# Optimization experiments

Measured on AMD Instinct MI355X. Metric: run time of the kernel, lower is better.

## Reference

```python
import jax, jax.numpy as jnp
import numpy as np

D_MODEL = 1024
NUM_HEADS = 16
KERNEL_EPS = 1e-4
NORM_STAB = 1e-6


def setup_inputs() -> dict:
    key = jax.random.key(0)
    k1, k2, k3, k4 = jax.random.split(key, 4)
    B, L = 4, 2048
    d_head, m = D_MODEL // NUM_HEADS, 256
    return {
        "query": jax.random.normal(k1, (B, L, D_MODEL), jnp.float32),
        "key": jax.random.normal(k2, (B, L, D_MODEL), jnp.float32),
        "value": jax.random.normal(k3, (B, L, D_MODEL), jnp.float32),
        # random projection matrix (fixed, not learned); original uses orthogonal blocks
        "random_features": jax.random.normal(k4, (d_head, m), jnp.float32),
    }


def _performer_forward(query, key, value, random_features):
    B, L, dm = query.shape
    h = NUM_HEADS
    d = dm // h
    m = random_features.shape[1]

    def split_heads(x):  # [B,L,dm] -> [B,h,L,d]
        return x.reshape(B, L, h, d).transpose(0, 2, 1, 3)

    q, k, v = split_heads(query), split_heads(key), split_heads(value)

    # FAVOR+ exp kernel with stabilizers (matches get_projected_queries_and_keys)
    scale = dm ** -0.25
    q = q * scale
    k = k * scale
    proj_q = jnp.einsum('bhld,dm->bhlm', q, random_features)
    proj_k = jnp.einsum('bhld,dm->bhlm', k, random_features)
    h_q = -0.5 * jnp.sum(q * q, axis=-1, keepdims=True)  # [B,h,L,1]
    h_k = -0.5 * jnp.sum(k * k, axis=-1, keepdims=True)
    q_stab = h_q  # reduce_max over a keepdims size-1 axis == identity (faithful)
    k_stab = jnp.max(h_k)  # global scalar
    q_kernel = jnp.exp(h_q + (proj_q - q_stab))
    k_kernel = jnp.exp(h_k + (proj_k - k_stab))
    nc = m ** -0.5
    q_prime = nc * (q_kernel + KERNEL_EPS)  # [B,h,L,m]
    k_prime = nc * (k_kernel + KERNEL_EPS)

    # Causal linear attention: streaming prefix state instead of [B,h,L,m,d] cumsum
    qp = q_prime.transpose(2, 0, 1, 3)  # [L,B,h,m]
    kp = k_prime.transpose(2, 0, 1, 3)
    vp = v.transpose(2, 0, 1, 3)        # [L,B,h,d]

    def step(carry, inp):
        S, Z = carry                      # S:[B,h,m,d], Z:[B,h,m]
        qt, kt, vt = inp
        S = S + kt[..., :, None] * vt[..., None, :]
        Z = Z + kt
        num = jnp.einsum('bhm,bhmd->bhd', qt, S)
        den = jnp.einsum('bhm,bhm->bh', qt, Z)
        return (S, Z), (num, den)

    S0 = jnp.zeros((B, h, m, d), q_prime.dtype)
    Z0 = jnp.zeros((B, h, m), q_prime.dtype)
    _, (nums, dens) = jax.lax.scan(step, (S0, Z0), (qp, kp, vp))
    nums = nums.transpose(1, 2, 0, 3)          # [B,h,L,d]
    dens = dens.transpose(1, 2, 0)[..., None]  # [B,h,L,1]

    # stabilize denominator near zero (matches _denominator_...)
    extreme = (jnp.abs(dens) <= NORM_STAB).astype(dens.dtype)
    dens = dens + 2.0 * NORM_STAB * extreme
    out = nums / dens

    # merge heads -> [B,L,dm]
    return out.transpose(0, 2, 1, 3).reshape(B, L, dm)


def reference(query, key, value, random_features):
    return _performer_forward(query, key, value, random_features)
```

## Files before the change

kernel.cpp:

```cpp
#include <hip/hip_runtime.h>


#define BB 4
#define HH 16
#define LL 2048
#define DH 64
#define DM 1024
#define MM 256
#define CC 64
#define NCH (LL / CC)

constexpr float SCALE = 0.17677669529663687f;
constexpr float NCF   = 0.0625f;
constexpr float KEPS  = 1e-4f;
constexpr float NCFK  = NCF * KEPS;
constexpr float NSTB  = 1e-6f;

typedef __attribute__((ext_vector_type(8))) short s16x8;
typedef __attribute__((ext_vector_type(4))) float f32x4;

__device__ __forceinline__ float bf2f(unsigned short s) {
  return __uint_as_float(((unsigned)s) << 16);
}
__device__ __forceinline__ unsigned short f2bf(float f) {
  unsigned u = __float_as_uint(f);
  u += 0x7FFFu + ((u >> 16) & 1u);
  return (unsigned short)(u >> 16);
}
__device__ __forceinline__ unsigned enc_key(float f) {
  unsigned u = __float_as_uint(f);
  return (u & 0x80000000u) ? ~u : (u | 0x80000000u);
}
__device__ __forceinline__ float dec_key(unsigned k) {
  unsigned u = (k & 0x80000000u) ? (k & 0x7FFFFFFFu) : ~k;
  return __uint_as_float(u);
}

__global__ __launch_bounds__(256) void kstab_kernel(const float* __restrict__ Kin,
                                                    unsigned int* __restrict__ wsu) {
  int lane = threadIdx.x & 63;
  int wave = threadIdx.x >> 6;
  int base = blockIdx.x * 64 + wave * 16;
  float m = -3.4e38f;
  for (int it = 0; it < 16; ++it) {
    int r = base + it;
    float v = Kin[(size_t)r * 64 + lane];
    float s = v * v;
    #pragma unroll
    for (int off = 32; off; off >>= 1) s += __shfl_xor(s, off, 64);
    float hk = -0.5f * (SCALE * SCALE) * s;
    m = fmaxf(m, hk);
  }
  __shared__ float wmax[4];
  if (lane == 0) wmax[wave] = m;
  __syncthreads();
  if (threadIdx.x == 0) {
    float mm = fmaxf(fmaxf(wmax[0], wmax[1]), fmaxf(wmax[2], wmax[3]));
    atomicMax(wsu, enc_key(mm));
  }
}

__global__ __launch_bounds__(256) void rft_prep(const float* __restrict__ RF,
                                                unsigned short* __restrict__ RFTg) {
  int m = threadIdx.x;
  float rv[64];
  #pragma unroll
  for (int d = 0; d < 64; ++d) rv[d] = RF[d * MM + m];
  unsigned swz = (unsigned)((m & 7) << 4);
  #pragma unroll
  for (int c16 = 0; c16 < 8; ++c16) {
    union { unsigned short u[8]; uint4 v; } pk_;
    #pragma unroll
    for (int i = 0; i < 8; ++i) pk_.u[i] = f2bf(rv[c16 * 8 + i]);
    unsigned byte = (unsigned)(m * 128) + (((unsigned)(c16 * 16)) ^ swz);
    *(uint4*)((char*)RFTg + byte) = pk_.v;
  }
}

__global__ __launch_bounds__(256) void phase1_kernel(const float* __restrict__ Kin,
                                                     const float* __restrict__ Vin,
                                                     const unsigned short* __restrict__ RFTg,
                                                     unsigned short* __restrict__ wsSb,
                                                     float* __restrict__ wsZ,
                                                     const unsigned int* __restrict__ wsu,
                                                     int bh0) {
  __shared__ __align__(16) char lds[45056];
  char* U0  = lds;
  char* KPl = lds + 16384;
  char* VT  = lds + 32768;
  float* Zw = (float*)(lds + 40960);

  int slice = blockIdx.x / NCH;
  int c     = blockIdx.x % NCH;
  int bh = bh0 + slice, b = bh >> 4, h = bh & 15;
  const int t    = threadIdx.x;
  const int lane = t & 63;
  const int w    = t >> 6;
  const int rloc = lane & 15;
  const int kc0  = (lane >> 4) * 8;
  const int arow = 16 * w + rloc;
  const unsigned lgrp16 = (unsigned)((lane >> 4) * 16);
  float kst = dec_key(*wsu);

  const float* krow = Kin + ((size_t)(b * LL + c * CC + arow)) * DM + h * DH;
  s16x8 kfrag[2];
  float ss = 0.f;
  #pragma unroll
  for (int kf = 0; kf < 2; ++kf) {
    float4 ka_ = *(const float4*)(krow + kf * 32 + kc0);
    float4 kb_ = *(const float4*)(krow + kf * 32 + kc0 + 4);
    float ks[8] = {ka_.x, ka_.y, ka_.z, ka_.w, kb_.x, kb_.y, kb_.z, kb_.w};
    #pragma unroll
    for (int i = 0; i < 8; ++i) {
      float kv = ks[i] * SCALE;
      ss += kv * kv;
      kfrag[kf][i] = (short)f2bf(kv);
    }
  }
  ss += __shfl_xor(ss, 16, 64);
  ss += __shfl_xor(ss, 32, 64);
  float hkv = -0.5f * ss;
  float hk4[4];
  #pragma unroll
  for (int r = 0; r < 4; ++r) hk4[r] = __shfl(hkv, (lane >> 4) * 4 + r, 64);

  {
    const float* vbase = Vin + ((size_t)(b * LL + c * CC + w * 16)) * DM + h * DH + lane;
    float vv[16];
    #pragma unroll
    for (int i = 0; i < 16; ++i) vv[i] = vbase[(size_t)i * DM];
    unsigned swz = (unsigned)((lane & 7) << 4);
    #pragma unroll
    for (int q = 0; q < 2; ++q) {
      union { unsigned short u[8]; uint4 v; } pk_;
      #pragma unroll
      for (int i = 0; i < 8; ++i) pk_.u[i] = f2bf(vv[q * 8 + i]);
      unsigned byte = (unsigned)(lane * 128) + (((unsigned)(w * 32 + q * 16)) ^ swz);
      *(uint4*)(VT + byte) = pk_.v;
    }
  }

  for (int h2 = 0; h2 < 2; ++h2) {
    __syncthreads();
    {
      const uint4* src = (const uint4*)(RFTg + (size_t)h2 * 8192);
      uint4* dst = (uint4*)U0;
      #pragma unroll
      for (int r2 = 0; r2 < 4; ++r2) dst[t + 256 * r2] = src[t + 256 * r2];
    }
    __syncthreads();

    f32x4 pk[8];
    #pragma unroll
    for (int i = 0; i < 8; ++i) pk[i] = (f32x4)0.f;
    #pragma unroll
    for (int mt = 0; mt < 8; ++mt) {
      int mloc = mt * 16 + rloc;
      unsigned rbyte = (unsigned)(mloc * 128);
      unsigned swz = (unsigned)((mloc & 7) << 4);
      #pragma unroll
      for (int kf = 0; kf < 2; ++kf) {
        s16x8 bf_ = *(const s16x8*)(U0 + rbyte + (((unsigned)(kf * 64) + lgrp16) ^ swz));
        pk[mt] = __builtin_amdgcn_mfma_f32_16x16x32_bf16(kfrag[kf], bf_, pk[mt], 0, 0, 0);
      }
    }
    #pragma unroll
    for (int mt = 0; mt < 8; ++mt) {
      int mloc = mt * 16 + rloc;
      float zp = 0.f;
      #pragma unroll
      for (int r = 0; r < 4; ++r) {
        int cpos = 16 * w + (lane >> 4) * 4 + r;
        float kpv = NCF * __expf(hk4[r] + pk[mt][r] - kst) + NCFK;
        zp += kpv;
        unsigned byte = (unsigned)(mloc * 128) +
                        (((unsigned)(cpos * 2)) ^ ((unsigned)((mloc & 7) << 4)));
        *(unsigned short*)(KPl + byte) = f2bf(kpv);
      }
      zp += __shfl_xor(zp, 16, 64);
      zp += __shfl_xor(zp, 32, 64);
      if (lane < 16) Zw[w * 256 + h2 * 128 + mt * 16 + lane] = zp;
    }
    __syncthreads();

    f32x4 sacc[8];
    #pragma unroll
    for (int i = 0; i < 8; ++i) sacc[i] = (f32x4)0.f;
    s16x8 af[2];
    {
      int drow = w * 16 + rloc;
      unsigned rbyte = (unsigned)(drow * 128);
      unsigned swz = (unsigned)((drow & 7) << 4);
      #pragma unroll
      for (int kf = 0; kf < 2; ++kf)
        af[kf] = *(const s16x8*)(VT + rbyte + (((unsigned)(kf * 64) + lgrp16) ^ swz));
    }
    #pragma unroll
    for (int mt = 0; mt < 8; ++mt) {
      int mrow = mt * 16 + rloc;
      unsigned rbyte = (unsigned)(mrow * 128);
      unsigned swz = (unsigned)((mrow & 7) << 4);
      #pragma unroll
      for (int kf = 0; kf < 2; ++kf) {
        s16x8 bf_ = *(const s16x8*)(KPl + rbyte + (((unsigned)(kf * 64) + lgrp16) ^ swz));
        sacc[mt] = __builtin_amdgcn_mfma_f32_16x16x32_bf16(af[kf], bf_, sacc[mt], 0, 0, 0);
      }
    }
    unsigned short* sdst = wsSb + (size_t)(slice * NCH + c) * 16384;
    #pragma unroll
    for (int mt = 0; mt < 8; ++mt) {
      #pragma unroll
      for (int r = 0; r < 4; ++r) {
        int d = w * 16 + (lane >> 4) * 4 + r;
        int m = h2 * 128 + mt * 16 + rloc;
        sdst[d * 256 + m] = f2bf(sacc[mt][r]);
      }
    }
  }
  __syncthreads();
  float z = Zw[t] + Zw[256 + t] + Zw[512 + t] + Zw[768 + t];
  wsZ[(size_t)(slice * NCH + c) * MM + t] = z;
}

__global__ __launch_bounds__(256) void scan_kernel(const unsigned short* __restrict__ wsSb,
                                                   unsigned short* __restrict__ wsPb,
                                                   float* __restrict__ wsZ) {
  int slice = blockIdx.x >> 3, part = blockIdx.x & 7;
  const int t = threadIdx.x;
  int d_l = t >> 5, moct = t & 31;
  int d = part * 8 + d_l, m0 = moct * 8;
  int half = m0 >> 7, m_l = m0 & 127;
  const unsigned short* srcb = wsSb + (size_t)slice * NCH * 16384 + d * 256 + m0;
  char* dstb = (char*)wsPb + ((size_t)slice * NCH * 2 + half) * 16384 +
               (unsigned)(d * 256) + (((unsigned)(m_l * 2)) ^ ((unsigned)((d & 7) << 4)));
  float run[8] = {0.f, 0.f, 0.f, 0.f, 0.f, 0.f, 0.f, 0.f};
  for (int c = 0; c < NCH; ++c) {
    uint4 v = *(const uint4*)(srcb + (size_t)c * 16384);
    union { unsigned short u[8]; uint4 q; } o;
    #pragma unroll
    for (int i = 0; i < 8; ++i) o.u[i] = f2bf(run[i]);
    *(uint4*)(dstb + (size_t)c * 32768) = o.q;
    const unsigned short* pv = (const unsigned short*)&v;
    #pragma unroll
    for (int i = 0; i < 8; ++i) run[i] += bf2f(pv[i]);
  }
  if (part == 0) {
    for (int e = t; e < MM; e += 256) {
      float zr = 0.f;
      for (int c = 0; c < NCH; ++c) {
        size_t idx = (size_t)slice * NCH * MM + (size_t)c * MM + e;
        float x = wsZ[idx];
        wsZ[idx] = zr;
        zr += x;
      }
    }
  }
}

__global__ __launch_bounds__(256) void phase3_kernel(const float* __restrict__ Qin,
                                                     const float* __restrict__ Kin,
                                                     const float* __restrict__ Vin,
                                                     const unsigned short* __restrict__ RFTg,
                                                     const unsigned short* __restrict__ wsPb,
                                                     const float* __restrict__ wsZ,
                                                     const unsigned int* __restrict__ wsu,
                                                     float* __restrict__ Out,
                                                     int bh0) {
  __shared__ __align__(16) char lds[50176];
  char* U0  = lds;
  char* QPl = lds + 16384;
  char* KPl = lds + 32768;
  float* ZL = (float*)(lds + 49152);

  int slice = blockIdx.x / NCH;
  int c     = blockIdx.x % NCH;
  int bh = bh0 + slice, b = bh >> 4, h = bh & 15;
  const int t    = threadIdx.x;
  const int lane = t & 63;
  const int w    = t >> 6;

  ZL[t] = wsZ[(size_t)(slice * NCH + c) * MM + t];
  float kst = dec_key(*wsu);

  const int rloc = lane & 15;
  const int kc0  = (lane >> 4) * 8;
  const int arow = 16 * w + rloc;
  const float* qrow = Qin + ((size_t)(b * LL + c * CC + arow)) * DM + h * DH;
  const float* krow = Kin + ((size_t)(b * LL + c * CC + arow)) * DM + h * DH;

  s16x8 qfrag[2], kfrag[2];
  float ss = 0.f;
  #pragma unroll
  for (int kf = 0; kf < 2; ++kf) {
    float4 qa_ = *(const float4*)(qrow + kf * 32 + kc0);
    float4 qb_ = *(const float4*)(qrow + kf * 32 + kc0 + 4);
    float4 ka_ = *(const float4*)(krow + kf * 32 + kc0);
    float4 kb_ = *(const float4*)(krow + kf * 32 + kc0 + 4);
    float qs[8] = {qa_.x, qa_.y, qa_.z, qa_.w, qb_.x, qb_.y, qb_.z, qb_.w};
    float ks[8] = {ka_.x, ka_.y, ka_.z, ka_.w, kb_.x, kb_.y, kb_.z, kb_.w};
    #pragma unroll
    for (int i = 0; i < 8; ++i) {
      float qv = qs[i] * SCALE, kv = ks[i] * SCALE;
      ss += kv * kv;
      qfrag[kf][i] = (short)f2bf(qv);
      kfrag[kf][i] = (short)f2bf(kv);
    }
  }
  ss += __shfl_xor(ss, 16, 64);
  ss += __shfl_xor(ss, 32, 64);
  float hkv = -0.5f * ss;

  f32x4 Aacc[4], Oacc[4];
  #pragma unroll
  for (int i = 0; i < 4; ++i) { Aacc[i] = (f32x4)0.f; Oacc[i] = (f32x4)0.f; }
  float den1[4] = {0.f, 0.f, 0.f, 0.f};
  float den2[4] = {0.f, 0.f, 0.f, 0.f};

  float hk4[4];
  #pragma unroll
  for (int r = 0; r < 4; ++r) hk4[r] = __shfl(hkv, (lane >> 4) * 4 + r, 64);

  const unsigned lgrp16 = (unsigned)((lane >> 4) * 16);

  for (int h2 = 0; h2 < 2; ++h2) {
    __syncthreads();
    {
      const uint4* src = (const uint4*)(RFTg + (size_t)h2 * 8192);
      uint4* dst = (uint4*)U0;
      #pragma unroll
      for (int r2 = 0; r2 < 4; ++r2) dst[t + 256 * r2] = src[t + 256 * r2];
    }
    __syncthreads();

    f32x4 pq[8], pk[8];
    #pragma unroll
    for (int i = 0; i < 8; ++i) { pq[i] = (f32x4)0.f; pk[i] = (f32x4)0.f; }
    #pragma unroll
    for (int mt = 0; mt < 8; ++mt) {
      int mloc = mt * 16 + rloc;
      unsigned rbyte = (unsigned)(mloc * 128);
      unsigned swz = (unsigned)((mloc & 7) << 4);
      #pragma unroll
      for (int kf = 0; kf < 2; ++kf) {
        s16x8 bf_ = *(const s16x8*)(U0 + rbyte + (((unsigned)(kf * 64) + lgrp16) ^ swz));
        pq[mt] = __builtin_amdgcn_mfma_f32_16x16x32_bf16(qfrag[kf], bf_, pq[mt], 0, 0, 0);
        pk[mt] = __builtin_amdgcn_mfma_f32_16x16x32_bf16(kfrag[kf], bf_, pk[mt], 0, 0, 0);
      }
    }
    #pragma unroll
    for (int mt = 0; mt < 8; ++mt) {
      int mloc = mt * 16 + rloc;
      #pragma unroll
      for (int r = 0; r < 4; ++r) {
        int row = 16 * w + (lane >> 4) * 4 + r;
        float qpv = NCF * __expf(pq[mt][r]) + NCFK;
        float kpv = NCF * __expf(hk4[r] + pk[mt][r] - kst) + NCFK;
        unsigned byte = (unsigned)(row * 256) +
                        (((unsigned)(mloc * 2)) ^ ((unsigned)((row & 7) << 4)));
        *(unsigned short*)(QPl + byte) = f2bf(qpv);
        *(unsigned short*)(KPl + byte) = f2bf(kpv);
        den2[r] += qpv * ZL[h2 * 128 + mloc];
      }
    }
    __syncthreads();

    uint4 stmp[4];
    {
      const char* ssrc = (const char*)wsPb + ((size_t)(slice * NCH + c) * 2 + h2) * 16384;
      #pragma unroll
      for (int r2 = 0; r2 < 4; ++r2)
        stmp[r2] = *(const uint4*)(ssrc + t * 16 + r2 * 4096);
    }

    s16x8 qa[4];
    {
      unsigned rbyte = (unsigned)(arow * 256);
      unsigned swz = (unsigned)((arow & 7) << 4);
      #pragma unroll
      for (int kf = 0; kf < 4; ++kf)
        qa[kf] = *(const s16x8*)(QPl + rbyte + (((unsigned)(kf * 64) + lgrp16) ^ swz));
    }
    for (int ct = 0; ct <= w; ++ct) {
      int rowb = ct * 16 + rloc;
      unsigned rbyte = (unsigned)(rowb * 256);
      unsigned swz = (unsigned)((rowb & 7) << 4);
      #pragma unroll
      for (int kf = 0; kf < 4; ++kf) {
        s16x8 bf_ = *(const s16x8*)(KPl + rbyte + (((unsigned)(kf * 64) + lgrp16) ^ swz));
        Aacc[ct] = __builtin_amdgcn_mfma_f32_16x16x32_bf16(qa[kf], bf_, Aacc[ct], 0, 0, 0);
      }
    }
    {
      uint4* u0v = (uint4*)U0;
      #pragma unroll
      for (int r2 = 0; r2 < 4; ++r2) u0v[t + 256 * r2] = stmp[r2];
    }
    __syncthreads();

    #pragma unroll
    for (int ct = 0; ct < 4; ++ct) {
      int rowb = ct * 16 + rloc;
      unsigned rbyte = (unsigned)(rowb * 256);
      unsigned swz = (unsigned)((rowb & 7) << 4);
      #pragma unroll
      for (int kf = 0; kf < 4; ++kf) {
        s16x8 bf_ = *(const s16x8*)(U0 + rbyte + (((unsigned)(kf * 64) + lgrp16) ^ swz));
        Oacc[ct] = __builtin_amdgcn_mfma_f32_16x16x32_bf16(qa[kf], bf_, Oacc[ct], 0, 0, 0);
      }
    }
  }

  __syncthreads();

  #pragma unroll
  for (int ct = 0; ct < 4; ++ct) {
    #pragma unroll
    for (int r = 0; r < 4; ++r) {
      int row = 16 * w + (lane >> 4) * 4 + r;
      int col = ct * 16 + rloc;
      float av = (ct <= w && col <= row) ? Aacc[ct][r] : 0.f;
      den1[r] += av;
      unsigned byte = (unsigned)(row * 128) +
                      (((unsigned)(col * 2)) ^ ((unsigned)((row & 7) << 4)));
      *(unsigned short*)(U0 + byte) = f2bf(av);
    }
  }
  {
    const float* vbase = Vin + ((size_t)(b * LL + c * CC + w * 16)) * DM + h * DH + lane;
    float vv[16];
    #pragma unroll
    for (int i = 0; i < 16; ++i) vv[i] = vbase[(size_t)i * DM];
    unsigned swz = (unsigned)((lane & 7) << 4);
    #pragma unroll
    for (int q = 0; q < 2; ++q) {
      union { unsigned short u[8]; uint4 v; } pk_;
      #pragma unroll
      for (int i = 0; i < 8; ++i) pk_.u[i] = f2bf(vv[q * 8 + i]);
      unsigned byte = 8192u + (unsigned)(lane * 128) + (((unsigned)(w * 32 + q * 16)) ^ swz);
      *(uint4*)(U0 + byte) = pk_.v;
    }
  }
  __syncthreads();

  {
    int nkf = (w >= 2) ? 2 : 1;
    unsigned arbyte = (unsigned)(arow * 128);
    unsigned aswz = (unsigned)((arow & 7) << 4);
    for (int kf = 0; kf < nkf; ++kf) {
      s16x8 af = *(const s16x8*)(U0 + arbyte + (((unsigned)(kf * 64) + lgrp16) ^ aswz));
      #pragma unroll
      for (int ct = 0; ct < 4; ++ct) {
        int rowv = ct * 16 + rloc;
        unsigned byte = 8192u + (unsigned)(rowv * 128) +
                        (((unsigned)(kf * 64) + lgrp16) ^ ((unsigned)((rowv & 7) << 4)));
        s16x8 vf = *(const s16x8*)(U0 + byte);
        Oacc[ct] = __builtin_amdgcn_mfma_f32_16x16x32_bf16(af, vf, Oacc[ct], 0, 0, 0);
      }
    }
  }

  float inv[4];
  #pragma unroll
  for (int r = 0; r < 4; ++r) {
    float dv = den1[r] + den2[r];
    dv += __shfl_xor(dv, 1, 64);
    dv += __shfl_xor(dv, 2, 64);
    dv += __shfl_xor(dv, 4, 64);
    dv += __shfl_xor(dv, 8, 64);
    if (fabsf(dv) <= NSTB) dv += 2.f * NSTB;
    inv[r] = 1.0f / dv;
  }
  #pragma unroll
  for (int r = 0; r < 4; ++r) {
    int row = 16 * w + (lane >> 4) * 4 + r;
    size_t g = ((size_t)(b * LL + c * CC + row)) * DM + h * DH;
    #pragma unroll
    for (int ct = 0; ct < 4; ++ct) {
      Out[g + ct * 16 + rloc] = Oacc[ct][r] * inv[r];
    }
  }
}

extern "C" void kernel_launch(void* const* d_in, const int* in_sizes, int n_in,
                              void* d_out, int out_size, void* d_ws, size_t ws_size,
                              hipStream_t stream) {
  const float* Q  = (const float*)d_in[0];
  const float* K  = (const float*)d_in[1];
  const float* V  = (const float*)d_in[2];
  const float* RF = (const float*)d_in[3];
  float* Out = (float*)d_out;
  unsigned int* wsu = (unsigned int*)d_ws;

  const size_t RESV = 1024;
  const size_t RFTB = 32768;
  const size_t perSlice = (size_t)NCH * 16384 * 2
                        + (size_t)NCH * 2 * 16384
                        + (size_t)NCH * MM * 4;
  int G = BB * HH;
  while (G > 1 && RESV + RFTB + (size_t)G * perSlice > ws_size) G >>= 1;

  unsigned short* RFTg = (unsigned short*)((char*)d_ws + RESV);
  unsigned short* wsSb = (unsigned short*)((char*)d_ws + RESV + RFTB);
  unsigned short* wsPb = wsSb + (size_t)G * NCH * 16384;
  float* wsZ = (float*)((char*)wsPb + (size_t)G * NCH * 2 * 16384);

  hipMemsetAsync(d_ws, 0, 4, stream);
  hipLaunchKernelGGL(kstab_kernel, dim3(2048), dim3(256), 0, stream, K, wsu);
  hipLaunchKernelGGL(rft_prep, dim3(1), dim3(256), 0, stream, RF, RFTg);
  for (int bh0 = 0; bh0 < BB * HH; bh0 += G) {
    hipLaunchKernelGGL(phase1_kernel, dim3(G * NCH), dim3(256), 0, stream,
                       K, V, RFTg, wsSb, wsZ, wsu, bh0);
    hipLaunchKernelGGL(scan_kernel, dim3(G * 8), dim3(256), 0, stream, wsSb, wsPb, wsZ);
    hipLaunchKernelGGL(phase3_kernel, dim3(G * NCH), dim3(256), 0, stream,
                       Q, K, V, RFTg, wsPb, wsZ, wsu, Out, bh0);
  }
}
```

Measured before the change: 163.5 us.

## Restructure chunked scan into 8-segment two-level prefix with in-block state carry

Phase 1 now processes four chunks per block and accumulates per-segment KV state in registers, writing one state per segment instead of one per chunk. The scan runs across only eight segments, and phase 3 carries the running state through its four chunks with in-register MFMA updates. The per-bh group loop is dropped, leaving a single launch of each kernel. This cuts workspace traffic and the size of the scan. In exchange, parallelism drops (448 and 512 blocks), phase 3 carries more work serially, and LDS per block is larger.

```diff
diff --git a/kernel.cpp b/kernel.cpp
--- a/kernel.cpp
+++ b/kernel.cpp
@@ -8,7 +8,9 @@
 #define DM 1024
 #define MM 256
 #define CC 64
-#define NCH (LL / CC)
+#define NCH 32
+#define SEGC 4
+#define NSEG 8
 
 constexpr float SCALE = 0.17677669529663687f;
 constexpr float NCF   = 0.0625f;
@@ -77,406 +79,441 @@
   }
 }
 
-__global__ __launch_bounds__(256) void phase1_kernel(const float* __restrict__ Kin,
-                                                     const float* __restrict__ Vin,
-                                                     const unsigned short* __restrict__ RFTg,
-                                                     unsigned short* __restrict__ wsSb,
-                                                     float* __restrict__ wsZ,
-                                                     const unsigned int* __restrict__ wsu,
-                                                     int bh0) {
-  __shared__ __align__(16) char lds[45056];
-  char* U0  = lds;
-  char* KPl = lds + 16384;
-  char* VT  = lds + 32768;
-  float* Zw = (float*)(lds + 40960);
-
-  int slice = blockIdx.x / NCH;
-  int c     = blockIdx.x % NCH;
-  int bh = bh0 + slice, b = bh >> 4, h = bh & 15;
-  const int t    = threadIdx.x;
-  const int lane = t & 63;
-  const int w    = t >> 6;
-  const int rloc = lane & 15;
-  const int kc0  = (lane >> 4) * 8;
+__global__ __launch_bounds__(256, 2) void phase1_kernel(const float* __restrict__ Kin,
+                                                        const float* __restrict__ Vin,
+                                                        const unsigned short* __restrict__ RFTg,
+                                                        unsigned short* __restrict__ wsSeg,
+                                                        float* __restrict__ wsZ,
+                                                        const unsigned int* __restrict__ wsu) {
+  __shared__ __align__(16) char lds[77824];
+  char* RFTl = lds;
+  char* KPmc = lds + 32768;
+  char* VT   = lds + 65536;
+  float* Zw  = (float*)(lds + 73728);
+
+  int slice = blockIdx.x / 7, seg = blockIdx.x % 7;
+  int b = slice >> 4, h = slice & 15;
+  const int t = threadIdx.x, lane = t & 63, w = t >> 6;
+  const int rloc = lane & 15, kc0 = (lane >> 4) * 8;
+  const unsigned lgrp16 = (unsigned)((lane >> 4) * 16);
+  float kst = dec_key(*wsu);
+
+  {
+    const uint4* src = (const uint4*)RFTg;
+    uint4* dst = (uint4*)RFTl;
+    #pragma unroll
+    for (int i = 0; i < 8; ++i) dst[t + 256 * i] = src[t + 256 * i];
+  }
+  #pragma unroll
+  for (int i = 0; i < 4; ++i) Zw[t + 256 * i] = 0.f;
+
+  f32x4 sacc[2][8];
+  #pragma unroll
+  for (int a = 0; a < 2; ++a)
+    #pragma unroll
+    for (int m = 0; m < 8; ++m) sacc[a][m] = (f32x4)0.f;
+
+  for (int cc = 0; cc < SEGC; ++cc) {
+    int c = seg * SEGC + cc;
+    const int arow = 16 * w + rloc;
+    const float* krow = Kin + ((size_t)(b * LL + c * CC + arow)) * DM + h * DH;
+    s16x8 kfrag[2];
+    float ss = 0.f;
+    #pragma unroll
+    for (int kf = 0; kf < 2; ++kf) {
+      float4 ka_ = *(const float4*)(krow + kf * 32 + kc0);
+      float4 kb_ = *(const float4*)(krow + kf * 32 + kc0 + 4);
+      float ks[8] = {ka_.x, ka_.y, ka_.z, ka_.w, kb_.x, kb_.y, kb_.z, kb_.w};
+      #pragma unroll
+      for (int i = 0; i < 8; ++i) {
+        float kv = ks[i] * SCALE;
+        ss += kv * kv;
+        kfrag[kf][i] = (short)f2bf(kv);
+      }
+    }
+    ss += __shfl_xor(ss, 16, 64);
+    ss += __shfl_xor(ss, 32, 64);
+    float hkv = -0.5f * ss;
+    float hk4[4];
+    #pragma unroll
+    for (int r = 0; r < 4; ++r) hk4[r] = __shfl(hkv, (lane >> 4) * 4 + r, 64);
+
+    const float* vbase = Vin + ((size_t)(b * LL + c * CC + w * 16)) * DM + h * DH + lane;
+    float vv[16];
+    #pragma unroll
+    for (int i = 0; i < 16; ++i) vv[i] = vbase[(size_t)i * DM];
+
+    __syncthreads();
+    {
+      unsigned vswz = (unsigned)((lane & 7) << 4);
+      #pragma unroll
+      for (int q = 0; q < 2; ++q) {
+        union { unsigned short u[8]; uint4 v; } pk_;
+        #pragma unroll
+        for (int i = 0; i < 8; ++i) pk_.u[i] = f2bf(vv[q * 8 + i]);
+        unsigned byte = (unsigned)(lane * 128) + (((unsigned)(w * 32 + q * 16)) ^ vswz);
+        *(uint4*)(VT + byte) = pk_.v;
+      }
+    }
+    __syncthreads();
+
+    #pragma unroll
+    for (int h2 = 0; h2 < 2; ++h2) {
+      #pragma unroll
+      for (int mt = 0; mt < 8; ++mt) {
+        int mloc = mt * 16 + rloc;
+        unsigned rbyte = (unsigned)((h2 * 128 + mloc) * 128);
+        unsigned swz = (unsigned)((mloc & 7) << 4);
+        f32x4 pk = (f32x4)0.f;
+        #pragma unroll
+        for (int kf = 0; kf < 2; ++kf) {
+          s16x8 bf_ = *(const s16x8*)(RFTl + rbyte + (((unsigned)(kf * 64) + lgrp16) ^ swz));
+          pk = __builtin_amdgcn_mfma_f32_16x16x32_bf16(kfrag[kf], bf_, pk, 0, 0, 0);
+        }
+        float zp = 0.f;
+        ushort4 kp4;
+        #pragma unroll
+        for (int r = 0; r < 4; ++r) {
+          float kpv = NCF * __expf(hk4[r] + pk[r] - kst) + NCFK;
+          zp += kpv;
+          (&kp4.x)[r] = f2bf(kpv);
+        }
+        int cb = 16 * w + (lane >> 4) * 4;
+        *(ushort4*)(KPmc + h2 * 16384 + mloc * 128 +
+                    (((unsigned)(cb * 2)) ^ ((unsigned)((mloc & 7) << 4)))) = kp4;
+        zp += __shfl_xor(zp, 16, 64);
+        zp += __shfl_xor(zp, 32, 64);
+        if (lane < 16) Zw[w * 256 + h2 * 128 + mt * 16 + lane] += zp;
+      }
+    }
+    __syncthreads();
+
+    s16x8 vt2[2];
+    {
+      int drow = w * 16 + rloc;
+      unsigned rb = (unsigned)(drow * 128), sz = (unsigned)((drow & 7) << 4);
+      #pragma unroll
+      for (int kf = 0; kf < 2; ++kf)
+        vt2[kf] = *(const s16x8*)(VT + rb + (((unsigned)(kf * 64) + lgrp16) ^ sz));
+    }
+    #pragma unroll
+    for (int h2 = 0; h2 < 2; ++h2) {
+      #pragma unroll
+      for (int mt = 0; mt < 8; ++mt) {
+        int mrow = mt * 16 + rloc;
+        unsigned rb = (unsigned)(h2 * 16384 + mrow * 128);
+        unsigned sz = (unsigned)((mrow & 7) << 4);
+        #pragma unroll
+        for (int kf = 0; kf < 2; ++kf) {
+          s16x8 bf_ = *(const s16x8*)(KPmc + rb + (((unsigned)(kf * 64) + lgrp16) ^ sz));
+          sacc[h2][mt] = __builtin_amdgcn_mfma_f32_16x16x32_bf16(vt2[kf], bf_, sacc[h2][mt], 0, 0, 0);
+        }
+      }
+    }
+  }
+
+  {
+    char* sb = (char*)wsSeg + (size_t)(slice * NSEG + seg) * 32768;
+    #pragma unroll
+    for (int j = 0; j < 8; ++j) {
+      int h2 = j >> 2, m0 = (j & 3) * 2;
+      union { unsigned short u[8]; uint4 v; } o;
+      #pragma unroll
+      for (int r = 0; r < 4; ++r) {
+        o.u[r]     = f2bf(sacc[h2][m0][r]);
+        o.u[4 + r] = f2bf(sacc[h2][m0 + 1][r]);
+      }
+      *(uint4*)(sb + (size_t)(j * 256 + t) * 16) = o.v;
+    }
+  }
+  __syncthreads();
+  float z = Zw[t] + Zw[256 + t] + Zw[512 + t] + Zw[768 + t];
+  wsZ[(size_t)(slice * NSEG + seg) * 256 + t] = z;
+}
+
+__global__ __launch_bounds__(256) void scan_kernel(unsigned short* __restrict__ wsSeg,
+                                                   float* __restrict__ wsZ) {
+  int slice = blockIdx.x >> 2, part = blockIdx.x & 3;
+  const int t = threadIdx.x;
+  #pragma unroll
+  for (int rep = 0; rep < 2; ++rep) {
+    int g = part * 512 + rep * 256 + t;
+    char* base = (char*)wsSeg + (size_t)slice * NSEG * 32768 + (size_t)g * 16;
+    float run[8] = {0.f, 0.f, 0.f, 0.f, 0.f, 0.f, 0.f, 0.f};
+    for (int s = 0; s < NSEG; ++s) {
+      char* p = base + (size_t)s * 32768;
+      uint4 x = make_uint4(0, 0, 0, 0);
+      if (s < NSEG - 1) x = *(const uint4*)p;
+      union { unsigned short u[8]; uint4 v; } o;
+      #pragma unroll
+      for (int i = 0; i < 8; ++i) o.u[i] = f2bf(run[i]);
+      *(uint4*)p = o.v;
+      const unsigned short* xu = (const unsigned short*)&x;
+      #pragma unroll
+      for (int i = 0; i < 8; ++i) run[i] += bf2f(xu[i]);
+    }
+  }
+  if (part == 0) {
+    float zr = 0.f;
+    for (int s = 0; s < NSEG; ++s) {
+      float* p = wsZ + ((size_t)slice * NSEG + s) * 256 + t;
+      float x = (s < NSEG - 1) ? *p : 0.f;
+      *p = zr;
+      zr += x;
+    }
+  }
+}
+
+__global__ __launch_bounds__(256, 2) void phase3_kernel(const float* __restrict__ Qin,
+                                                        const float* __restrict__ Kin,
+                                                        const float* __restrict__ Vin,
+                                                        const unsigned short* __restrict__ RFTg,
+                                                        const unsigned short* __restrict__ wsSeg,
+                                                        const float* __restrict__ wsZ,
+                                                        const unsigned int* __restrict__ wsu,
+                                                        float* __restrict__ Out) {
+  __shared__ __align__(16) char lds[78848];
+  char* U0   = lds;
+  char* QP   = lds + 16384;
+  char* KPcm = lds + 32768;
+  char* KPmc = lds + 49152;
+  char* VT   = lds + 65536;
+  float* Zw  = (float*)(lds + 73728);
+  float* ZL  = (float*)(lds + 77824);
+
+  int slice = blockIdx.x >> 3, seg = blockIdx.x & 7;
+  int b = slice >> 4, h = slice & 15;
+  const int t = threadIdx.x, lane = t & 63, w = t >> 6;
+  const int rloc = lane & 15, kc0 = (lane >> 4) * 8;
   const int arow = 16 * w + rloc;
   const unsigned lgrp16 = (unsigned)((lane >> 4) * 16);
   float kst = dec_key(*wsu);
-
-  const float* krow = Kin + ((size_t)(b * LL + c * CC + arow)) * DM + h * DH;
-  s16x8 kfrag[2];
-  float ss = 0.f;
-  #pragma unroll
-  for (int kf = 0; kf < 2; ++kf) {
-    float4 ka_ = *(const float4*)(krow + kf * 32 + kc0);
-    float4 kb_ = *(const float4*)(krow + kf * 32 + kc0 + 4);
-    float ks[8] = {ka_.x, ka_.y, ka_.z, ka_.w, kb_.x, kb_.y, kb_.z, kb_.w};
-    #pragma unroll
-    for (int i = 0; i < 8; ++i) {
-      float kv = ks[i] * SCALE;
-      ss += kv * kv;
-      kfrag[kf][i] = (short)f2bf(kv);
-    }
-  }
-  ss += __shfl_xor(ss, 16, 64);
-  ss += __shfl_xor(ss, 32, 64);
-  float hkv = -0.5f * ss;
-  float hk4[4];
-  #pragma unroll
-  for (int r = 0; r < 4; ++r) hk4[r] = __shfl(hkv, (lane >> 4) * 4 + r, 64);
-
+  int slab = slice * NSEG + seg;
+
+  ZL[t] = wsZ[(size_t)slab * 256 + t];
+
+  f32x4 sacc[2][8];
   {
+    const char* sb = (const char*)wsSeg + (size_t)slab * 32768;
+    #pragma unroll
+    for (int j = 0; j < 8; ++j) {
+      uint4 x = *(const uint4*)(sb + (size_t)(j * 256 + t) * 16);
+      const unsigned short* xu = (const unsigned short*)&x;
+      int h2 = j >> 2, m0 = (j & 3) * 2;
+      #pragma unroll
+      for (int r = 0; r < 4; ++r) {
+        sacc[h2][m0][r]     = bf2f(xu[r]);
+        sacc[h2][m0 + 1][r] = bf2f(xu[4 + r]);
+      }
+    }
+  }
+
+  for (int cc = 0; cc < SEGC; ++cc) {
+    int c = seg * SEGC + cc;
+    const float* qrow = Qin + ((size_t)(b * LL + c * CC + arow)) * DM + h * DH;
+    const float* krow = Kin + ((size_t)(b * LL + c * CC + arow)) * DM + h * DH;
+    s16x8 qfrag[2], kfrag[2];
+    float ss = 0.f;
+    #pragma unroll
+    for (int kf = 0; kf < 2; ++kf) {
+      float4 qa_ = *(const float4*)(qrow + kf * 32 + kc0);
+      float4 qb_ = *(const float4*)(qrow + kf * 32 + kc0 + 4);
+      float4 ka_ = *(const float4*)(krow + kf * 32 + kc0);
+      float4 kb_ = *(const float4*)(krow + kf * 32 + kc0 + 4);
+      float qs[8] = {qa_.x, qa_.y, qa_.z, qa_.w, qb_.x, qb_.y, qb_.z, qb_.w};
+      float ks[8] = {ka_.x, ka_.y, ka_.z, ka_.w, kb_.x, kb_.y, kb_.z, kb_.w};
+      #pragma unroll
+      for (int i = 0; i < 8; ++i) {
+        float qv = qs[i] * SCALE, kv = ks[i] * SCALE;
+        ss += kv * kv;
+        qfrag[kf][i] = (short)f2bf(qv);
+        kfrag[kf][i] = (short)f2bf(kv);
+      }
+    }
+    ss += __shfl_xor(ss, 16, 64);
+    ss += __shfl_xor(ss, 32, 64);
+    float hkv = -0.5f * ss;
+    float hk4[4];
+    #pragma unroll
+    for (int r = 0; r < 4; ++r) hk4[r] = __shfl(hkv, (lane >> 4) * 4 + r, 64);
+
     const float* vbase = Vin + ((size_t)(b * LL + c * CC + w * 16)) * DM + h * DH + lane;
     float vv[16];
     #pragma unroll
     for (int i = 0; i < 16; ++i) vv[i] = vbase[(size_t)i * DM];
-    unsigned swz = (unsigned)((lane & 7) << 4);
-    #pragma unroll
-    for (int q = 0; q < 2; ++q) {
-      union { unsigned short u[8]; uint4 v; } pk_;
-      #pragma unroll
-      for (int i = 0; i < 8; ++i) pk_.u[i] = f2bf(vv[q * 8 + i]);
-      unsigned byte = (unsigned)(lane * 128) + (((unsigned)(w * 32 + q * 16)) ^ swz);
-      *(uint4*)(VT + byte) = pk_.v;
-    }
-  }
-
-  for (int h2 = 0; h2 < 2; ++h2) {
+
+    f32x4 Aacc[4], Oacc[4];
+    #pragma unroll
+    for (int i = 0; i < 4; ++i) { Aacc[i] = (f32x4)0.f; Oacc[i] = (f32x4)0.f; }
+    float den1[4] = {0.f, 0.f, 0.f, 0.f};
+    float den2[4] = {0.f, 0.f, 0.f, 0.f};
+
+    for (int h2 = 0; h2 < 2; ++h2) {
+      __syncthreads();
+      if (h2 == 0) {
+        unsigned vswz = (unsigned)((lane & 7) << 4);
+        #pragma unroll
+        for (int q = 0; q < 2; ++q) {
+          union { unsigned short u[8]; uint4 v; } pk_;
+          #pragma unroll
+          for (int i = 0; i < 8; ++i) pk_.u[i] = f2bf(vv[q * 8 + i]);
+          unsigned byte = (unsigned)(lane * 128) + (((unsigned)(w * 32 + q * 16)) ^ vswz);
+          *(uint4*)(VT + byte) = pk_.v;
+        }
+      }
+      {
+        const uint4* src = (const uint4*)RFTg + h2 * 1024;
+        uint4* dst = (uint4*)U0;
+        #pragma unroll
+        for (int i = 0; i < 4; ++i) dst[t + 256 * i] = src[t + 256 * i];
+      }
+      __syncthreads();
+
+      #pragma unroll
+      for (int mt = 0; mt < 8; ++mt) {
+        int mloc = mt * 16 + rloc;
+        unsigned rbyte = (unsigned)(mloc * 128);
+        unsigned swz = (unsigned)((mloc & 7) << 4);
+        f32x4 pq = (f32x4)0.f, pk = (f32x4)0.f;
+        #pragma unroll
+        for (int kf = 0; kf < 2; ++kf) {
+          s16x8 bf_ = *(const s16x8*)(U0 + rbyte + (((unsigned)(kf * 64) + lgrp16) ^ swz));
+          pq = __builtin_amdgcn_mfma_f32_16x16x32_bf16(qfrag[kf], bf_, pq, 0, 0, 0);
+          pk = __builtin_amdgcn_mfma_f32_16x16x32_bf16(kfrag[kf], bf_, pk, 0, 0, 0);
+        }
+        float zlv = ZL[h2 * 128 + mloc];
+        float zp = 0.f;
+        ushort4 kp4;
+        #pragma unroll
+        for (int r = 0; r < 4; ++r) {
+          int row = 16 * w + (lane >> 4) * 4 + r;
+          float qpv = NCF * __expf(pq[r]) + NCFK;
+          float kpv = NCF * __expf(hk4[r] + pk[r] - kst) + NCFK;
+          den2[r] += qpv * zlv;
+          zp += kpv;
+          (&kp4.x)[r] = f2bf(kpv);
+          unsigned rswz = (unsigned)((row & 7) << 4);
+          *(unsigned short*)(QP + row * 256 + (((unsigned)(mloc * 2)) ^ rswz)) = f2bf(qpv);
+          *(unsigned short*)(KPcm + row * 256 + (((unsigned)(mloc * 2)) ^ rswz)) = f2bf(kpv);
+        }
+        int cb = 16 * w + (lane >> 4) * 4;
+        *(ushort4*)(KPmc + mloc * 128 + (((unsigned)(cb * 2)) ^ ((unsigned)((mloc & 7) << 4)))) = kp4;
+        zp += __shfl_xor(zp, 16, 64);
+        zp += __shfl_xor(zp, 32, 64);
+        if (lane < 16) Zw[w * 256 + h2 * 128 + mt * 16 + lane] = zp;
+      }
+      __syncthreads();
+
+      s16x8 qa[4];
+      {
+        unsigned rb = (unsigned)(arow * 256), sz = (unsigned)((arow & 7) << 4);
+        #pragma unroll
+        for (int kf = 0; kf < 4; ++kf)
+          qa[kf] = *(const s16x8*)(QP + rb + (((unsigned)(kf * 64) + lgrp16) ^ sz));
+      }
+      for (int ct = 0; ct <= w; ++ct) {
+        int rowb = ct * 16 + rloc;
+        unsigned rb = (unsigned)(rowb * 256), sz = (unsigned)((rowb & 7) << 4);
+        #pragma unroll
+        for (int kf = 0; kf < 4; ++kf) {
+          s16x8 bf_ = *(const s16x8*)(KPcm + rb + (((unsigned)(kf * 64) + lgrp16) ^ sz));
+          Aacc[ct] = __builtin_amdgcn_mfma_f32_16x16x32_bf16(qa[kf], bf_, Aacc[ct], 0, 0, 0);
+        }
+      }
+      #pragma unroll
+      for (int mt = 0; mt < 8; ++mt) {
+        int mloc = mt * 16 + rloc;
+        #pragma unroll
+        for (int r = 0; r < 4; ++r) {
+          int d = 16 * w + (lane >> 4) * 4 + r;
+          *(unsigned short*)(U0 + d * 256 +
+                             (((unsigned)(mloc * 2)) ^ ((unsigned)((d & 7) << 4)))) =
+              f2bf(sacc[h2][mt][r]);
+        }
+      }
+      if (cc != SEGC - 1) {
+        s16x8 vt2[2];
+        {
+          int drow = w * 16 + rloc;
+          unsigned rb = (unsigned)(drow * 128), sz = (unsigned)((drow & 7) << 4);
+          #pragma unroll
+          for (int kf = 0; kf < 2; ++kf)
+            vt2[kf] = *(const s16x8*)(VT + rb + (((unsigned)(kf * 64) + lgrp16) ^ sz));
+        }
+        #pragma unroll
+        for (int mt = 0; mt < 8; ++mt) {
+          int mrow = mt * 16 + rloc;
+          unsigned rb = (unsigned)(mrow * 128), sz = (unsigned)((mrow & 7) << 4);
+          #pragma unroll
+          for (int kf = 0; kf < 2; ++kf) {
+            s16x8 bf_ = *(const s16x8*)(KPmc + rb + (((unsigned)(kf * 64) + lgrp16) ^ sz));
+            sacc[h2][mt] = __builtin_amdgcn_mfma_f32_16x16x32_bf16(vt2[kf], bf_, sacc[h2][mt], 0, 0, 0);
+          }
+        }
+      }
+      __syncthreads();
+      #pragma unroll
+      for (int ct = 0; ct < 4; ++ct) {
+        int rowb = ct * 16 + rloc;
+        unsigned rb = (unsigned)(rowb * 256), sz = (unsigned)((rowb & 7) << 4);
+        #pragma unroll
+        for (int kf = 0; kf < 4; ++kf) {
+          s16x8 bf_ = *(const s16x8*)(U0 + rb + (((unsigned)(kf * 64) + lgrp16) ^ sz));
+          Oacc[ct] = __builtin_amdgcn_mfma_f32_16x16x32_bf16(qa[kf], bf_, Oacc[ct], 0, 0, 0);
+        }
+      }
+    }
+
     __syncthreads();
-    {
-      const uint4* src = (const uint4*)(RFTg + (size_t)h2 * 8192);
-      uint4* dst = (uint4*)U0;
-      #pragma unroll
-      for (int r2 = 0; r2 < 4; ++r2) dst[t + 256 * r2] = src[t + 256 * r2];
-    }
-    __syncthreads();
-
-    f32x4 pk[8];
-    #pragma unroll
-    for (int i = 0; i < 8; ++i) pk[i] = (f32x4)0.f;
-    #pragma unroll
-    for (int mt = 0; mt < 8; ++mt) {
-      int mloc = mt * 16 + rloc;
-      unsigned rbyte = (unsigned)(mloc * 128);
-      unsigned swz = (unsigned)((mloc & 7) << 4);
-      #pragma unroll
-      for (int kf = 0; kf < 2; ++kf) {
-        s16x8 bf_ = *(const s16x8*)(U0 + rbyte + (((unsigned)(kf * 64) + lgrp16) ^ swz));
-        pk[mt] = __builtin_amdgcn_mfma_f32_16x16x32_bf16(kfrag[kf], bf_, pk[mt], 0, 0, 0);
-      }
-    }
-    #pragma unroll
-    for (int mt = 0; mt < 8; ++mt) {
-      int mloc = mt * 16 + rloc;
-      float zp = 0.f;
-      #pragma unroll
-      for (int r = 0; r < 4; ++r) {
-        int cpos = 16 * w + (lane >> 4) * 4 + r;
-        float kpv = NCF * __expf(hk4[r] + pk[mt][r] - kst) + NCFK;
-        zp += kpv;
-        unsigned byte = (unsigned)(mloc * 128) +
-                        (((unsigned)(cpos * 2)) ^ ((unsigned)((mloc & 7) << 4)));
-        *(unsigned short*)(KPl + byte) = f2bf(kpv);
-      }
-      zp += __shfl_xor(zp, 16, 64);
-      zp += __shfl_xor(zp, 32, 64);
-      if (lane < 16) Zw[w * 256 + h2 * 128 + mt * 16 + lane] = zp;
-    }
-    __syncthreads();
-
-    f32x4 sacc[8];
-    #pragma unroll
-    for (int i = 0; i < 8; ++i) sacc[i] = (f32x4)0.f;
-    s16x8 af[2];
-    {
-      int drow = w * 16 + rloc;
-      unsigned rbyte = (unsigned)(drow * 128);
-      unsigned swz = (unsigned)((drow & 7) << 4);
-      #pragma unroll
-      for (int kf = 0; kf < 2; ++kf)
-        af[kf] = *(const s16x8*)(VT + rbyte + (((unsigned)(kf * 64) + lgrp16) ^ swz));
-    }
-    #pragma unroll
-    for (int mt = 0; mt < 8; ++mt) {
-      int mrow = mt * 16 + rloc;
-      unsigned rbyte = (unsigned)(mrow * 128);
-      unsigned swz = (unsigned)((mrow & 7) << 4);
-      #pragma unroll
-      for (int kf = 0; kf < 2; ++kf) {
-        s16x8 bf_ = *(const s16x8*)(KPl + rbyte + (((unsigned)(kf * 64) + lgrp16) ^ swz));
-        sacc[mt] = __builtin_amdgcn_mfma_f32_16x16x32_bf16(af[kf], bf_, sacc[mt], 0, 0, 0);
-      }
-    }
-    unsigned short* sdst = wsSb + (size_t)(slice * NCH + c) * 16384;
-    #pragma unroll
-    for (int mt = 0; mt < 8; ++mt) {
-      #pragma unroll
-      for (int r = 0; r < 4; ++r) {
-        int d = w * 16 + (lane >> 4) * 4 + r;
-        int m = h2 * 128 + mt * 16 + rloc;
-        sdst[d * 256 + m] = f2bf(sacc[mt][r]);
-      }
-    }
-  }
-  __syncthreads();
-  float z = Zw[t] + Zw[256 + t] + Zw[512 + t] + Zw[768 + t];
-  wsZ[(size_t)(slice * NCH + c) * MM + t] = z;
-}
-
-__global__ __launch_bounds__(256) void scan_kernel(const unsigned short* __restrict__ wsSb,
-                                                   unsigned short* __restrict__ wsPb,
-                                                   float* __restrict__ wsZ) {
-  int slice = blockIdx.x >> 3, part = blockIdx.x & 7;
-  const int t = threadIdx.x;
-  int d_l = t >> 5, moct = t & 31;
-  int d = part * 8 + d_l, m0 = moct * 8;
-  int half = m0 >> 7, m_l = m0 & 127;
-  const unsigned short* srcb = wsSb + (size_t)slice * NCH * 16384 + d * 256 + m0;
-  char* dstb = (char*)wsPb + ((size_t)slice * NCH * 2 + half) * 16384 +
-               (unsigned)(d * 256) + (((unsigned)(m_l * 2)) ^ ((unsigned)((d & 7) << 4)));
-  float run[8] = {0.f, 0.f, 0.f, 0.f, 0.f, 0.f, 0.f, 0.f};
-  for (int c = 0; c < NCH; ++c) {
-    uint4 v = *(const uint4*)(srcb + (size_t)c * 16384);
-    union { unsigned short u[8]; uint4 q; } o;
-    #pragma unroll
-    for (int i = 0; i < 8; ++i) o.u[i] = f2bf(run[i]);
-    *(uint4*)(dstb + (size_t)c * 32768) = o.q;
-    const unsigned short* pv = (const unsigned short*)&v;
-    #pragma unroll
-    for (int i = 0; i < 8; ++i) run[i] += bf2f(pv[i]);
-  }
-  if (part == 0) {
-    for (int e = t; e < MM; e += 256) {
-      float zr = 0.f;
-      for (int c = 0; c < NCH; ++c) {
-        size_t idx = (size_t)slice * NCH * MM + (size_t)c * MM + e;
-        float x = wsZ[idx];
-        wsZ[idx] = zr;
-        zr += x;
-      }
-    }
-  }
-}
-
-__global__ __launch_bounds__(256) void phase3_kernel(const float* __restrict__ Qin,
-                                                     const float* __restrict__ Kin,
-                                                     const float* __restrict__ Vin,
-                                                     const unsigned short* __restrict__ RFTg,
-                                                     const unsigned short* __restrict__ wsPb,
-                                                     const float* __restrict__ wsZ,
-                                                     const unsigned int* __restrict__ wsu,
-                                                     float* __restrict__ Out,
-                                                     int bh0) {
-  __shared__ __align__(16) char lds[50176];
-  char* U0  = lds;
-  char* QPl = lds + 16384;
-  char* KPl = lds + 32768;
-  float* ZL = (float*)(lds + 49152);
-
-  int slice = blockIdx.x / NCH;
-  int c     = blockIdx.x % NCH;
-  int bh = bh0 + slice, b = bh >> 4, h = bh & 15;
-  const int t    = threadIdx.x;
-  const int lane = t & 63;
-  const int w    = t >> 6;
-
-  ZL[t] = wsZ[(size_t)(slice * NCH + c) * MM + t];
-  float kst = dec_key(*wsu);
-
-  const int rloc = lane & 15;
-  const int kc0  = (lane >> 4) * 8;
-  const int arow = 16 * w + rloc;
-  const float* qrow = Qin + ((size_t)(b * LL + c * CC + arow)) * DM + h * DH;
-  const float* krow = Kin + ((size_t)(b * LL + c * CC + arow)) * DM + h * DH;
-
-  s16x8 qfrag[2], kfrag[2];
-  float ss = 0.f;
-  #pragma unroll
-  for (int kf = 0; kf < 2; ++kf) {
-    float4 qa_ = *(const float4*)(qrow + kf * 32 + kc0);
-    float4 qb_ = *(const float4*)(qrow + kf * 32 + kc0 + 4);
-    float4 ka_ = *(const float4*)(krow + kf * 32 + kc0);
-    float4 kb_ = *(const float4*)(krow + kf * 32 + kc0 + 4);
-    float qs[8] = {qa_.x, qa_.y, qa_.z, qa_.w, qb_.x, qb_.y, qb_.z, qb_.w};
-    float ks[8] = {ka_.x, ka_.y, ka_.z, ka_.w, kb_.x, kb_.y, kb_.z, kb_.w};
-    #pragma unroll
-    for (int i = 0; i < 8; ++i) {
-      float qv = qs[i] * SCALE, kv = ks[i] * SCALE;
-      ss += kv * kv;
-      qfrag[kf][i] = (short)f2bf(qv);
-      kfrag[kf][i] = (short)f2bf(kv);
-    }
-  }
-  ss += __shfl_xor(ss, 16, 64);
-  ss += __shfl_xor(ss, 32, 64);
-  float hkv = -0.5f * ss;
-
-  f32x4 Aacc[4], Oacc[4];
-  #pragma unroll
-  for (int i = 0; i < 4; ++i) { Aacc[i] = (f32x4)0.f; Oacc[i] = (f32x4)0.f; }
-  float den1[4] = {0.f, 0.f, 0.f, 0.f};
-  float den2[4] = {0.f, 0.f, 0.f, 0.f};
-
-  float hk4[4];
-  #pragma unroll
-  for (int r = 0; r < 4; ++r) hk4[r] = __shfl(hkv, (lane >> 4) * 4 + r, 64);
-
-  const unsigned lgrp16 = (unsigned)((lane >> 4) * 16);
-
-  for (int h2 = 0; h2 < 2; ++h2) {
-    __syncthreads();
-    {
-      const uint4* src = (const uint4*)(RFTg + (size_t)h2 * 8192);
-      uint4* dst = (uint4*)U0;
-      #pragma unroll
-      for (int r2 = 0; r2 < 4; ++r2) dst[t + 256 * r2] = src[t + 256 * r2];
-    }
-    __syncthreads();
-
-    f32x4 pq[8], pk[8];
-    #pragma unroll
-    for (int i = 0; i < 8; ++i) { pq[i] = (f32x4)0.f; pk[i] = (f32x4)0.f; }
-    #pragma unroll
-    for (int mt = 0; mt < 8; ++mt) {
-      int mloc = mt * 16 + rloc;
-      unsigned rbyte = (unsigned)(mloc * 128);
-      unsigned swz = (unsigned)((mloc & 7) << 4);
-      #pragma unroll
-      for (int kf = 0; kf < 2; ++kf) {
-        s16x8 bf_ = *(const s16x8*)(U0 + rbyte + (((unsigned)(kf * 64) + lgrp16) ^ swz));
-        pq[mt] = __builtin_amdgcn_mfma_f32_16x16x32_bf16(qfrag[kf], bf_, pq[mt], 0, 0, 0);
-        pk[mt] = __builtin_amdgcn_mfma_f32_16x16x32_bf16(kfrag[kf], bf_, pk[mt], 0, 0, 0);
-      }
-    }
-    #pragma unroll
-    for (int mt = 0; mt < 8; ++mt) {
-      int mloc = mt * 16 + rloc;
+    #pragma unroll
+    for (int ct = 0; ct < 4; ++ct) {
       #pragma unroll
       for (int r = 0; r < 4; ++r) {
         int row = 16 * w + (lane >> 4) * 4 + r;
-        float qpv = NCF * __expf(pq[mt][r]) + NCFK;
-        float kpv = NCF * __expf(hk4[r] + pk[mt][r] - kst) + NCFK;
-        unsigned byte = (unsigned)(row * 256) +
-                        (((unsigned)(mloc * 2)) ^ ((unsigned)((row & 7) << 4)));
-        *(unsigned short*)(QPl + byte) = f2bf(qpv);
-        *(unsigned short*)(KPl + byte) = f2bf(kpv);
-        den2[r] += qpv * ZL[h2 * 128 + mloc];
-      }
-    }
+        int col = ct * 16 + rloc;
+        float av = (ct <= w && col <= row) ? Aacc[ct][r] : 0.f;
+        den1[r] += av;
+        *(unsigned short*)(U0 + row * 128 +
+                           (((unsigned)(col * 2)) ^ ((unsigned)((row & 7) << 4)))) = f2bf(av);
+      }
+    }
+    if (cc != SEGC - 1) ZL[t] += Zw[t] + Zw[256 + t] + Zw[512 + t] + Zw[768 + t];
     __syncthreads();
 
-    uint4 stmp[4];
     {
-      const char* ssrc = (const char*)wsPb + ((size_t)(slice * NCH + c) * 2 + h2) * 16384;
-      #pragma unroll
-      for (int r2 = 0; r2 < 4; ++r2)
-        stmp[r2] = *(const uint4*)(ssrc + t * 16 + r2 * 4096);
-    }
-
-    s16x8 qa[4];
-    {
-      unsigned rbyte = (unsigned)(arow * 256);
-      unsigned swz = (unsigned)((arow & 7) << 4);
-      #pragma unroll
-      for (int kf = 0; kf < 4; ++kf)
-        qa[kf] = *(const s16x8*)(QPl + rbyte + (((unsigned)(kf * 64) + lgrp16) ^ swz));
-    }
-    for (int ct = 0; ct <= w; ++ct) {
-      int rowb = ct * 16 + rloc;
-      unsigned rbyte = (unsigned)(rowb * 256);
-      unsigned swz = (unsigned)((rowb & 7) << 4);
-      #pragma unroll
-      for (int kf = 0; kf < 4; ++kf) {
-        s16x8 bf_ = *(const s16x8*)(KPl + rbyte + (((unsigned)(kf * 64) + lgrp16) ^ swz));
-        Aacc[ct] = __builtin_amdgcn_mfma_f32_16x16x32_bf16(qa[kf], bf_, Aacc[ct], 0, 0, 0);
-      }
-    }
-    {
-      uint4* u0v = (uint4*)U0;
-      #pragma unroll
-      for (int r2 = 0; r2 < 4; ++r2) u0v[t + 256 * r2] = stmp[r2];
-    }
-    __syncthreads();
-
-    #pragma unroll
-    for (int ct = 0; ct < 4; ++ct) {
-      int rowb = ct * 16 + rloc;
-      unsigned rbyte = (unsigned)(rowb * 256);
-      unsigned swz = (unsigned)((rowb & 7) << 4);
-      #pragma unroll
-      for (int kf = 0; kf < 4; ++kf) {
-        s16x8 bf_ = *(const s16x8*)(U0 + rbyte + (((unsigned)(kf * 64) + lgrp16) ^ swz));
-        Oacc[ct] = __builtin_amdgcn_mfma_f32_16x16x32_bf16(qa[kf], bf_, Oacc[ct], 0, 0, 0);
-      }
-    }
-  }
-
-  __syncthreads();
-
-  #pragma unroll
-  for (int ct = 0; ct < 4; ++ct) {
+      int nkf = (w >= 2) ? 2 : 1;
+      unsigned arb = (unsigned)(arow * 128), asz = (unsigned)((arow & 7) << 4);
+      for (int kf = 0; kf < nkf; ++kf) {
+        s16x8 af = *(const s16x8*)(U0 + arb + (((unsigned)(kf * 64) + lgrp16) ^ asz));
+        #pragma unroll
+        for (int ct = 0; ct < 4; ++ct) {
+          int rowv = ct * 16 + rloc;
+          s16x8 vf = *(const s16x8*)(VT + rowv * 128 +
+                                     (((unsigned)(kf * 64) + lgrp16) ^ ((unsigned)((rowv & 7) << 4))));
+          Oacc[ct] = __builtin_amdgcn_mfma_f32_16x16x32_bf16(af, vf, Oacc[ct], 0, 0, 0);
+        }
+      }
+    }
+
+    float inv[4];
+    #pragma unroll
+    for (int r = 0; r < 4; ++r) {
+      float dv = den1[r] + den2[r];
+      dv += __shfl_xor(dv, 1, 64);
+      dv += __shfl_xor(dv, 2, 64);
+      dv += __shfl_xor(dv, 4, 64);
+      dv += __shfl_xor(dv, 8, 64);
+      if (fabsf(dv) <= NSTB) dv += 2.f * NSTB;
+      inv[r] = 1.0f / dv;
+    }
     #pragma unroll
     for (int r = 0; r < 4; ++r) {
       int row = 16 * w + (lane >> 4) * 4 + r;
-      int col = ct * 16 + rloc;
-      float av = (ct <= w && col <= row) ? Aacc[ct][r] : 0.f;
-      den1[r] += av;
-      unsigned byte = (unsigned)(row * 128) +
-                      (((unsigned)(col * 2)) ^ ((unsigned)((row & 7) << 4)));
-      *(unsigned short*)(U0 + byte) = f2bf(av);
-    }
-  }
-  {
-    const float* vbase = Vin + ((size_t)(b * LL + c * CC + w * 16)) * DM + h * DH + lane;
-    float vv[16];
-    #pragma unroll
-    for (int i = 0; i < 16; ++i) vv[i] = vbase[(size_t)i * DM];
-    unsigned swz = (unsigned)((lane & 7) << 4);
-    #pragma unroll
-    for (int q = 0; q < 2; ++q) {
-      union { unsigned short u[8]; uint4 v; } pk_;
-      #pragma unroll
-      for (int i = 0; i < 8; ++i) pk_.u[i] = f2bf(vv[q * 8 + i]);
-      unsigned byte = 8192u + (unsigned)(lane * 128) + (((unsigned)(w * 32 + q * 16)) ^ swz);
-      *(uint4*)(U0 + byte) = pk_.v;
-    }
-  }
-  __syncthreads();
-
-  {
-    int nkf = (w >= 2) ? 2 : 1;
-    unsigned arbyte = (unsigned)(arow * 128);
-    unsigned aswz = (unsigned)((arow & 7) << 4);
-    for (int kf = 0; kf < nkf; ++kf) {
-      s16x8 af = *(const s16x8*)(U0 + arbyte + (((unsigned)(kf * 64) + lgrp16) ^ aswz));
+      size_t g = ((size_t)(b * LL + c * CC + row)) * DM + h * DH;
       #pragma unroll
       for (int ct = 0; ct < 4; ++ct) {
-        int rowv = ct * 16 + rloc;
-        unsigned byte = 8192u + (unsigned)(rowv * 128) +
-                        (((unsigned)(kf * 64) + lgrp16) ^ ((unsigned)((rowv & 7) << 4)));
-        s16x8 vf = *(const s16x8*)(U0 + byte);
-        Oacc[ct] = __builtin_amdgcn_mfma_f32_16x16x32_bf16(af, vf, Oacc[ct], 0, 0, 0);
-      }
-    }
-  }
-
-  float inv[4];
-  #pragma unroll
-  for (int r = 0; r < 4; ++r) {
-    float dv = den1[r] + den2[r];
-    dv += __shfl_xor(dv, 1, 64);
-    dv += __shfl_xor(dv, 2, 64);
-    dv += __shfl_xor(dv, 4, 64);
-    dv += __shfl_xor(dv, 8, 64);
-    if (fabsf(dv) <= NSTB) dv += 2.f * NSTB;
-    inv[r] = 1.0f / dv;
-  }
-  #pragma unroll
-  for (int r = 0; r < 4; ++r) {
-    int row = 16 * w + (lane >> 4) * 4 + r;
-    size_t g = ((size_t)(b * LL + c * CC + row)) * DM + h * DH;
-    #pragma unroll
-    for (int ct = 0; ct < 4; ++ct) {
-      Out[g + ct * 16 + rloc] = Oacc[ct][r] * inv[r];
+        Out[g + ct * 16 + rloc] = Oacc[ct][r] * inv[r];
+      }
     }
   }
 }
@@ -493,25 +530,16 @@
 
   const size_t RESV = 1024;
   const size_t RFTB = 32768;
-  const size_t perSlice = (size_t)NCH * 16384 * 2
-                        + (size_t)NCH * 2 * 16384
-                        + (size_t)NCH * MM * 4;
-  int G = BB * HH;
-  while (G > 1 && RESV + RFTB + (size_t)G * perSlice > ws_size) G >>= 1;
-
-  unsigned short* RFTg = (unsigned short*)((char*)d_ws + RESV);
-  unsigned short* wsSb = (unsigned short*)((char*)d_ws + RESV + RFTB);
-  unsigned short* wsPb = wsSb + (size_t)G * NCH * 16384;
-  float* wsZ = (float*)((char*)wsPb + (size_t)G * NCH * 2 * 16384);
+  unsigned short* RFTg  = (unsigned short*)((char*)d_ws + RESV);
+  unsigned short* wsSeg = (unsigned short*)((char*)d_ws + RESV + RFTB);
+  float* wsZ = (float*)((char*)d_ws + RESV + RFTB + (size_t)64 * NSEG * 32768);
 
   hipMemsetAsync(d_ws, 0, 4, stream);
   hipLaunchKernelGGL(kstab_kernel, dim3(2048), dim3(256), 0, stream, K, wsu);
   hipLaunchKernelGGL(rft_prep, dim3(1), dim3(256), 0, stream, RF, RFTg);
-  for (int bh0 = 0; bh0 < BB * HH; bh0 += G) {
-    hipLaunchKernelGGL(phase1_kernel, dim3(G * NCH), dim3(256), 0, stream,
-                       K, V, RFTg, wsSb, wsZ, wsu, bh0);
-    hipLaunchKernelGGL(scan_kernel, dim3(G * 8), dim3(256), 0, stream, wsSb, wsPb, wsZ);
-    hipLaunchKernelGGL(phase3_kernel, dim3(G * NCH), dim3(256), 0, stream,
-                       Q, K, V, RFTg, wsPb, wsZ, wsu, Out, bh0);
-  }
-}
+  hipLaunchKernelGGL(phase1_kernel, dim3(64 * 7), dim3(256), 0, stream,
+                     K, V, RFTg, wsSeg, wsZ, wsu);
+  hipLaunchKernelGGL(scan_kernel, dim3(256), dim3(256), 0, stream, wsSeg, wsZ);
+  hipLaunchKernelGGL(phase3_kernel, dim3(64 * NSEG), dim3(256), 0, stream,
+                     Q, K, V, RFTg, wsSeg, wsZ, wsu, Out);
+}
```

Result: slower. 183.8 us (+12.4%).
